# Performance work log

Hardware: AMD Instinct MI355X
Metric: run time of the kernel (lower is better)

The kernel has to match this reference:

```python
import jax, jax.numpy as jnp
import numpy as np

EPS = 1e-08
BASE_CR = 0.5
MIN_CR = 0.1


def _layernorm(h, g, b, eps=1e-5):
    m = jnp.mean(h, axis=-1, keepdims=True)
    v = jnp.mean((h - m) ** 2, axis=-1, keepdims=True)
    return (h - m) * jax.lax.rsqrt(v + eps) * g + b


def _normalize(h, eps=1e-12):
    n = jnp.sqrt(jnp.sum(h * h, axis=-1, keepdims=True))
    return h / jnp.maximum(n, eps)


def _conv1d(h, w, b):
    # h: [B,S,D], w: [K,I,O] (WIO), cross-correlation, SAME padding (torch Conv1d padding=1, k=3)
    y = jax.lax.conv_general_dilated(h, w, window_strides=(1,), padding='SAME',
                                     dimension_numbers=('NWC', 'WIO', 'NWC'))
    return y + b


def setup_inputs() -> dict:
    key = jax.random.key(0)
    ks = jax.random.split(key, 8)
    V, L, D, B, S = 50257, 2048, 1024, 8, 2048
    inp = {
        'x': jax.random.randint(ks[0], (B, S), 0, V),
        'token_emb': jax.random.normal(ks[1], (V, D), jnp.float32) * 0.02,
        'pos_emb': jax.random.normal(ks[2], (L, D), jnp.float32) * 0.02,
        'conv1_w': jax.random.normal(ks[3], (3, D, D), jnp.float32) * 0.025,
        'conv1_b': jnp.zeros((D,), jnp.float32),
        'conv2_w': jax.random.normal(ks[4], (3, D, D), jnp.float32) * 0.025,
        'conv2_b': jnp.zeros((D,), jnp.float32),
        'proj_w': jax.random.normal(ks[5], (D, D), jnp.float32) * 0.03,
        'proj_b': jnp.zeros((D,), jnp.float32),
        'ph_w': jax.random.normal(ks[6], (D, D), jnp.float32) * 0.03,
        'ph_b': jnp.zeros((D,), jnp.float32),
        'ln_g': jnp.ones((D,), jnp.float32),
        'ln_b': jnp.zeros((D,), jnp.float32),
    }
    return inp


def reference(x, token_emb, pos_emb, conv1_w, conv1_b, conv2_w, conv2_b,
              proj_w, proj_b, ph_w, ph_b, ln_g, ln_b):
    B, S = x.shape
    # token + position embedding
    h = token_emb[x] + pos_emb[:S][None, :, :]                 # [B,S,D]
    # two conv1d + gelu (exact erf, matching torch F.gelu default)
    h = jax.nn.gelu(_conv1d(h, conv1_w, conv1_b), approximate=False)
    h = jax.nn.gelu(_conv1d(h, conv2_w, conv2_b), approximate=False)
    h = _layernorm(h, ln_g, ln_b)
    # dropout is identity in eval mode
    # S is a power of two -> next_power_of_two(S) == S, no padding
    x_fft = jnp.fft.fft(h, axis=1)                              # [B,S,D] complex64
    magnitude = jnp.abs(x_fft)
    thresh = 0.1 * jnp.max(magnitude, axis=1, keepdims=True)
    complexity = jnp.mean((magnitude > thresh).astype(jnp.float32), axis=(1, 2))  # [B]
    cr = jnp.clip(BASE_CR * (1.0 - complexity), MIN_CR, 1.0)
    N = jnp.clip((cr * S).astype(jnp.int32), 1, S)              # [B] kept coefficients
    # vectorized ragged masking (replaces per-sample python loop/scatter)
    mask = (jnp.arange(S)[None, :] < N[:, None]).astype(jnp.float32)   # [B,S]
    x_fft_c = x_fft * mask[:, :, None]
    x_ifft_raw = jnp.fft.ifft(x_fft_c, n=S, axis=1).real        # [B,S,D]
    proj_out = x_ifft_raw @ proj_w + proj_b
    x_ifft = _layernorm(proj_out, ln_g, ln_b)
    recon_target = proj_out                                     # same proj of same ifft
    # loss
    cos_sim = jnp.sum(_normalize(x_ifft) * _normalize(recon_target), axis=-1)
    cos_sim = jnp.clip(cos_sim, -1.0 + EPS, 1.0 - EPS)
    d = x_ifft - recon_target
    l1 = jnp.where(jnp.abs(d) < 1.0, 0.5 * d * d, jnp.abs(d) - 0.5)    # smooth_l1, beta=1
    proj_x = x_ifft @ ph_w + ph_b
    proj_t = recon_target @ ph_w + ph_b
    sem = jnp.mean((_normalize(proj_x) - _normalize(proj_t)) ** 2, axis=-1)  # [B,S]
    combined = 0.6 * jnp.mean(1.0 - cos_sim) + 0.2 * jnp.mean(l1, axis=-1) + 0.2 * sem
    loss = jnp.sum(combined * mask) / (jnp.sum(mask) + EPS)
    return (x_ifft, loss)
```

## Files before the change

### kernel.cpp

```cpp
#include <hip/hip_runtime.h>
#include <math.h>

#define S_LEN 2048
#define D_DIM 1024
#define B_BATCH 8
#define R_ROWS (B_BATCH * S_LEN)
#define BD_ROWS (B_BATCH * D_DIM)
#define PAD_ROWS 2050

typedef unsigned short u16;
typedef unsigned int u32;
typedef __attribute__((ext_vector_type(8))) short bf16x8;
typedef __attribute__((ext_vector_type(4))) float f32x4;

__device__ __forceinline__ u16 f2bf(float f) {
    u32 x = __float_as_uint(f);
    u32 r = (x + 0x7fffu + ((x >> 16) & 1u)) >> 16;
    return (u16)r;
}
__device__ __forceinline__ float bf2f(u16 u) {
    return __uint_as_float(((u32)u) << 16);
}
__device__ __forceinline__ float gelu_exact(float x) {
    return 0.5f * x * (1.0f + erff(x * 0.70710678118654752f));
}
__device__ __forceinline__ int dr4(int v) {
    v = __brev((unsigned)v) >> 22;
    return ((v & 0x155) << 1) | ((v >> 1) & 0x155);
}
#define PIDX(i) ((i) + ((i) >> 5))

#define GLDS(gsrc, ldst)                                                                   \
    __builtin_amdgcn_global_load_lds(                                                      \
        (const __attribute__((address_space(1))) u32*)(gsrc),                              \
        (__attribute__((address_space(3))) u32*)(ldst), 16, 0, 0)

#define WAIT_LGKM0 do { asm volatile("s_waitcnt lgkmcnt(0)" ::: "memory");                 \
                        __builtin_amdgcn_sched_barrier(0); } while (0)
#define WAIT_VM(n)   do { asm volatile("s_waitcnt vmcnt(" #n ")" ::: "memory");            \
                          __builtin_amdgcn_sched_barrier(0); } while (0)

__global__ __launch_bounds__(256) void zero_pads(u16* __restrict__ P0, u16* __restrict__ P1)
{
    const int bid = blockIdx.x;
    u16* P = (bid >= 16) ? P1 : P0;
    const int ridx = bid & 15;
    const int b = ridx >> 1;
    const size_t row = (size_t)b * PAD_ROWS + (size_t)(ridx & 1) * (PAD_ROWS - 1);
    ((uint2*)(P + row * D_DIM))[threadIdx.x] = make_uint2(0u, 0u);
}

__global__ __launch_bounds__(256) void wconv(const float* __restrict__ W, u16* __restrict__ WT)
{
    __shared__ float t[32][33];
    const int tap = blockIdx.z;
    const int n0 = blockIdx.x * 32, k0 = blockIdx.y * 32;
    const int tx = threadIdx.x, ty = threadIdx.y;
    const float* ip = W + (size_t)tap * D_DIM * D_DIM;
    u16* op = WT + (size_t)tap * D_DIM * D_DIM;
#pragma unroll
    for (int u = 0; u < 4; u++)
        t[ty + u * 8][tx] = ip[(size_t)(k0 + ty + u * 8) * D_DIM + n0 + tx];
    __syncthreads();
#pragma unroll
    for (int u = 0; u < 4; u++)
        op[(size_t)(n0 + ty + u * 8) * D_DIM + k0 + tx] = f2bf(t[tx][ty + u * 8]);
}

__global__ __launch_bounds__(256) void wconv_inter(
    const float* __restrict__ W, const float* __restrict__ g, u16* __restrict__ WTI)
{
    __shared__ float t[32][33];
    const int n0 = blockIdx.x * 32, k0 = blockIdx.y * 32;
    const int tx = threadIdx.x, ty = threadIdx.y;
#pragma unroll
    for (int u = 0; u < 4; u++)
        t[ty + u * 8][tx] = W[(size_t)(k0 + ty + u * 8) * D_DIM + n0 + tx];
    __syncthreads();
    const float gk = g[k0 + tx];
#pragma unroll
    for (int u = 0; u < 4; u++) {
        const int n = n0 + ty + u * 8;
        const float w = t[tx][ty + u * 8];
        WTI[((size_t)(2 * n) << 10) + k0 + tx] = f2bf(w);
        WTI[((size_t)(2 * n + 1) << 10) + k0 + tx] = f2bf(w * gk);
    }
}

__global__ __launch_bounds__(256) void gemv_ph(
    const u16* __restrict__ WTI, const float* __restrict__ lnb,
    const float* __restrict__ phb, float* __restrict__ vg, float* __restrict__ c0)
{
    const int wid = threadIdx.x >> 6, lane = threadIdx.x & 63;
    const int n = blockIdx.x * 4 + wid;
    const u16* r0 = WTI + ((size_t)(2 * n) << 10) + lane * 16;
    const u16* r1 = WTI + ((size_t)(2 * n + 1) << 10) + lane * 16;
    float sb = 0.f, sg = 0.f;
#pragma unroll
    for (int h = 0; h < 2; h++) {
        uint4 w0 = *(const uint4*)(r0 + h * 8);
        uint4 w1 = *(const uint4*)(r1 + h * 8);
        float a[8], b8[8];
        a[0] = bf2f((u16)(w0.x & 0xffff)); a[1] = bf2f((u16)(w0.x >> 16));
        a[2] = bf2f((u16)(w0.y & 0xffff)); a[3] = bf2f((u16)(w0.y >> 16));
        a[4] = bf2f((u16)(w0.z & 0xffff)); a[5] = bf2f((u16)(w0.z >> 16));
        a[6] = bf2f((u16)(w0.w & 0xffff)); a[7] = bf2f((u16)(w0.w >> 16));
        b8[0] = bf2f((u16)(w1.x & 0xffff)); b8[1] = bf2f((u16)(w1.x >> 16));
        b8[2] = bf2f((u16)(w1.y & 0xffff)); b8[3] = bf2f((u16)(w1.y >> 16));
        b8[4] = bf2f((u16)(w1.z & 0xffff)); b8[5] = bf2f((u16)(w1.z >> 16));
        b8[6] = bf2f((u16)(w1.w & 0xffff)); b8[7] = bf2f((u16)(w1.w >> 16));
        const int kb = lane * 16 + h * 8;
        float4 l0 = *(const float4*)(lnb + kb), l1 = *(const float4*)(lnb + kb + 4);
        sb += a[0]*l0.x + a[1]*l0.y + a[2]*l0.z + a[3]*l0.w
            + a[4]*l1.x + a[5]*l1.y + a[6]*l1.z + a[7]*l1.w;
        sg += b8[0] + b8[1] + b8[2] + b8[3] + b8[4] + b8[5] + b8[6] + b8[7];
    }
#pragma unroll
    for (int off = 32; off > 0; off >>= 1) {
        sg += __shfl_xor(sg, off);
        sb += __shfl_xor(sb, off);
    }
    if (lane == 0) { vg[n] = sg; c0[n] = sb + phb[n]; }
}

__global__ __launch_bounds__(256) void emb_kernel(
    const int* __restrict__ x, const float* __restrict__ tok,
    const float* __restrict__ pos, u16* __restrict__ P0)
{
    const int row = blockIdx.x;
    const int tid = threadIdx.x;
    const int t = x[row];
    const int s = row & (S_LEN - 1);
    const int b = row >> 11;
    float4 a = ((const float4*)(tok + (size_t)t * D_DIM))[tid];
    float4 p = ((const float4*)(pos + (size_t)s * D_DIM))[tid];
    uint2 v;
    v.x = (u32)f2bf(a.x + p.x) | ((u32)f2bf(a.y + p.y) << 16);
    v.y = (u32)f2bf(a.z + p.z) | ((u32)f2bf(a.w + p.w) << 16);
    ((uint2*)(P0 + ((size_t)b * PAD_ROWS + 1 + s) * D_DIM))[tid] = v;
}

__global__ __launch_bounds__(512, 2) void gemm_8ph(
    const u16* __restrict__ A, const u16* __restrict__ WT,
    const float* __restrict__ bias,
    float* __restrict__ outF, u16* __restrict__ outB,
    int ntaps, int doGelu, int aPadded, int outBPadded)
{
    __shared__ u16 As[2][2][8192];
    __shared__ u16 Bs[2][2][8192];
    const int tid = threadIdx.x;
    const int wid = tid >> 6, lane = tid & 63;
    const int wm = wid >> 2, wn = wid & 3;
    const int l15 = lane & 15, l4 = lane >> 4;
    const int flat = blockIdx.y * 4 + blockIdx.x;
    const int xcd = flat & 7;
    const int ii = flat >> 3;
    const int by = xcd * 8 + (ii >> 2);
    const int bx = ii & 3;
    const int row0 = by * 256;
    const int col0 = bx * 256;
    const int b = row0 >> 11;
    const int srow0 = row0 & (S_LEN - 1);
    const int nt = ntaps * 16;
    const int NI = nt >> 1;

    const int stR = tid >> 2;
    const int stKc = (((tid & 3) ^ ((tid >> 3) & 3)) << 3);
    const int ldsOff = tid * 16;
    const int swz4 = ((l4 ^ ((l15 >> 1) & 3)) << 4);

#define STAGE_A(T_, s_) do {                                                               \
        const int tap_ = (T_) >> 4;                                                        \
        const int kb_ = ((T_) & 15) * 64 + (s_) * 32 + stKc;                               \
        const size_t ar_ = (aPadded ? (size_t)(b * PAD_ROWS + srow0 + tap_)                \
                                    : (size_t)row0);                                       \
        GLDS(A + ((ar_ + stR) << 10) + kb_,                                                \
             (char*)&As[(T_) & 1][s_][0] + ldsOff);                                        \
        GLDS(A + ((ar_ + stR + 128) << 10) + kb_,                                          \
             (char*)&As[(T_) & 1][s_][0] + ldsOff + 8192);                                 \
    } while (0)
#define STAGE_B(T_, s_) do {                                                               \
        const int tap_ = (T_) >> 4;                                                        \
        const int kb_ = ((T_) & 15) * 64 + (s_) * 32 + stKc;                               \
        const u16* wp_ = WT + ((size_t)tap_ << 20) + ((size_t)(col0 + stR) << 10) + kb_;   \
        GLDS(wp_, (char*)&Bs[(T_) & 1][s_][0] + ldsOff);                                   \
        GLDS(wp_ + (size_t)(128 << 10), (char*)&Bs[(T_) & 1][s_][0] + ldsOff + 8192);      \
    } while (0)
#define RD_A(dst_, buf_, s_, mih_) do {                                                    \
        const char* p_ = (const char*)&As[buf_][s_][0]                                     \
                         + (size_t)(wm * 128 + (mih_) * 64 + l15) * 64 + swz4;             \
        dst_[0] = *(const bf16x8*)(p_);                                                    \
        dst_[1] = *(const bf16x8*)(p_ + 1024);                                             \
        dst_[2] = *(const bf16x8*)(p_ + 2048);                                             \
        dst_[3] = *(const bf16x8*)(p_ + 3072);                                             \
    } while (0)
#define RD_B(dst_, buf_, s_) do {                                                          \
        const char* p_ = (const char*)&Bs[buf_][s_][0]                                     \
                         + (size_t)(wn * 64 + l15) * 64 + swz4;                            \
        dst_[0] = *(const bf16x8*)(p_);                                                    \
        dst_[1] = *(const bf16x8*)(p_ + 1024);                                             \
        dst_[2] = *(const bf16x8*)(p_ + 2048);                                             \
        dst_[3] = *(const bf16x8*)(p_ + 3072);                                             \
    } while (0)
#define MF(mih_, av_, bv_) do {                                                            \
        __builtin_amdgcn_s_setprio(1);                                                     \
        _Pragma("unroll")                                                                  \
        for (int mi_ = 0; mi_ < 4; mi_++)                                                  \
            _Pragma("unroll")                                                              \
            for (int ni_ = 0; ni_ < 4; ni_++)                                              \
                acc[(mih_) * 4 + mi_][ni_] = __builtin_amdgcn_mfma_f32_16x16x32_bf16(      \
                    av_[mi_], bv_[ni_], acc[(mih_) * 4 + mi_][ni_], 0, 0, 0);              \
        __builtin_amdgcn_s_setprio(0);                                                     \
    } while (0)
#define BAR __builtin_amdgcn_s_barrier()

    f32x4 acc[8][4];
#pragma unroll
    for (int m = 0; m < 8; m++)
#pragma unroll
        for (int n = 0; n < 4; n++) acc[m][n] = (f32x4){0.f, 0.f, 0.f, 0.f};

    STAGE_A(0, 0); STAGE_B(0, 0);
    STAGE_A(0, 1); STAGE_B(0, 1);
    STAGE_A(1, 0); STAGE_B(1, 0);
    WAIT_VM(4);
    BAR;

    for (int i = 0; i < NI; ++i) {
        const int o = 2 * i + 1;
        const int e2 = 2 * i + 2, o2 = 2 * i + 3;
        const bool last = (i == NI - 1);
        bf16x8 a[4], bv[4];
        RD_A(a, 0, 0, 0); RD_B(bv, 0, 0);
        STAGE_A(o, 1);
        BAR; WAIT_LGKM0;
        MF(0, a, bv);
        BAR;
        RD_A(a, 0, 0, 1);
        STAGE_B(o, 1);
        BAR; WAIT_LGKM0;
        MF(1, a, bv);
        BAR;
        RD_A(a, 0, 1, 0); RD_B(bv, 0, 1);
        if (!last) STAGE_A(e2, 0);
        BAR; WAIT_LGKM0;
        MF(0, a, bv);
        BAR;
        RD_A(a, 0, 1, 1);
        if (!last) STAGE_B(e2, 0);
        BAR; WAIT_LGKM0;
        MF(1, a, bv);
        if (last) { WAIT_VM(0); } else { WAIT_VM(4); }
        BAR;
        RD_A(a, 1, 0, 0); RD_B(bv, 1, 0);
        if (!last) STAGE_A(e2, 1);
        BAR; WAIT_LGKM0;
        MF(0, a, bv);
        BAR;
        RD_A(a, 1, 0, 1);
        if (!last) STAGE_B(e2, 1);
        BAR; WAIT_LGKM0;
        MF(1, a, bv);
        BAR;
        RD_A(a, 1, 1, 0); RD_B(bv, 1, 1);
        if (!last) STAGE_A(o2, 0);
        BAR; WAIT_LGKM0;
        MF(0, a, bv);
        BAR;
        RD_A(a, 1, 1, 1);
        if (!last) STAGE_B(o2, 0);
        BAR; WAIT_LGKM0;
        MF(1, a, bv);
        if (!last) { WAIT_VM(4); }
        BAR;
    }
#undef STAGE_A

    float bb[4];
#pragma unroll
    for (int ni = 0; ni < 4; ni++) bb[ni] = bias[col0 + wn * 64 + ni * 16 + l15];

#pragma unroll
    for (int mi = 0; mi < 8; mi++) {
#pragma unroll
        for (int ni = 0; ni < 4; ni++) {
#pragma unroll
            for (int reg = 0; reg < 4; reg++) {
                const int row = row0 + wm * 128 + mi * 16 + l4 * 4 + reg;
                const int col = col0 + wn * 64 + ni * 16 + l15;
                float v = acc[mi][ni][reg] + bb[ni];
                if (doGelu) v = gelu_exact(v);
                if (outF) outF[(size_t)row * D_DIM + col] = v;
                if (outB) {
                    const size_t orow = outBPadded
                        ? ((size_t)(row >> 11) * PAD_ROWS + 1 + (size_t)(row & (S_LEN - 1)))
                        : (size_t)row;
                    outB[orow * D_DIM + col] = f2bf(v);
                }
            }
        }
    }
}

__global__ __launch_bounds__(512, 2) void phstats_8ph(
    const u16* __restrict__ A, const u16* __restrict__ WTI,
    const float* __restrict__ phb, const float* __restrict__ vg,
    const float* __restrict__ c0, const float2* __restrict__ stats2,
    float* __restrict__ Sxx, float* __restrict__ Stt, float* __restrict__ Sxt)
{
    __shared__ u16 As[2][2][8192];
    __shared__ u16 Bs[2][2][8192];
    const int tid = threadIdx.x;
    const int wid = tid >> 6, lane = tid & 63;
    const int wm = wid >> 2, wn = wid & 3;
    const int l15 = lane & 15, l4 = lane >> 4;
    const int flat = blockIdx.y * 8 + blockIdx.x;
    const int xcd = flat & 7;
    const int ii = flat >> 3;
    const int by = xcd * 8 + (ii >> 3);
    const int bx = ii & 7;
    const int row0 = by * 256;
    const int col0 = bx * 256;
    const int NI = 8;

    const int stR = tid >> 2;
    const int stKc = (((tid & 3) ^ ((tid >> 3) & 3)) << 3);
    const int ldsOff = tid * 16;
    const int swz4 = ((l4 ^ ((l15 >> 1) & 3)) << 4);

#define STAGE_A(T_, s_) do {                                                               \
        const int kb_ = ((T_) & 15) * 64 + (s_) * 32 + stKc;                               \
        GLDS(A + (((size_t)row0 + stR) << 10) + kb_,                                       \
             (char*)&As[(T_) & 1][s_][0] + ldsOff);                                        \
        GLDS(A + (((size_t)row0 + stR + 128) << 10) + kb_,                                 \
             (char*)&As[(T_) & 1][s_][0] + ldsOff + 8192);                                 \
    } while (0)
#define STAGE_BI(T_, s_) do {                                                              \
        const int kb_ = ((T_) & 15) * 64 + (s_) * 32 + stKc;                               \
        const u16* wp_ = WTI + ((size_t)(col0 + stR) << 10) + kb_;                         \
        GLDS(wp_, (char*)&Bs[(T_) & 1][s_][0] + ldsOff);                                   \
        GLDS(wp_ + (size_t)(128 << 10), (char*)&Bs[(T_) & 1][s_][0] + ldsOff + 8192);      \
    } while (0)

    f32x4 acc[8][4];
#pragma unroll
    for (int m = 0; m < 8; m++)
#pragma unroll
        for (int n = 0; n < 4; n++) acc[m][n] = (f32x4){0.f, 0.f, 0.f, 0.f};

    STAGE_A(0, 0); STAGE_BI(0, 0);
    STAGE_A(0, 1); STAGE_BI(0, 1);
    STAGE_A(1, 0); STAGE_BI(1, 0);
    WAIT_VM(4);
    BAR;

    for (int i = 0; i < NI; ++i) {
        const int o = 2 * i + 1;
        const int e2 = 2 * i + 2, o2 = 2 * i + 3;
        const bool last = (i == NI - 1);
        bf16x8 a[4], bv[4];
        RD_A(a, 0, 0, 0); RD_B(bv, 0, 0);
        STAGE_A(o, 1);
        BAR; WAIT_LGKM0;
        MF(0, a, bv);
        BAR;
        RD_A(a, 0, 0, 1);
        STAGE_BI(o, 1);
        BAR; WAIT_LGKM0;
        MF(1, a, bv);
        BAR;
        RD_A(a, 0, 1, 0); RD_B(bv, 0, 1);
        if (!last) STAGE_A(e2, 0);
        BAR; WAIT_LGKM0;
        MF(0, a, bv);
        BAR;
        RD_A(a, 0, 1, 1);
        if (!last) STAGE_BI(e2, 0);
        BAR; WAIT_LGKM0;
        MF(1, a, bv);
        if (last) { WAIT_VM(0); } else { WAIT_VM(4); }
        BAR;
        RD_A(a, 1, 0, 0); RD_B(bv, 1, 0);
        if (!last) STAGE_A(e2, 1);
        BAR; WAIT_LGKM0;
        MF(0, a, bv);
        BAR;
        RD_A(a, 1, 0, 1);
        if (!last) STAGE_BI(e2, 1);
        BAR; WAIT_LGKM0;
        MF(1, a, bv);
        BAR;
        RD_A(a, 1, 1, 0); RD_B(bv, 1, 1);
        if (!last) STAGE_A(o2, 0);
        BAR; WAIT_LGKM0;
        MF(0, a, bv);
        BAR;
        RD_A(a, 1, 1, 1);
        if (!last) STAGE_BI(o2, 0);
        BAR; WAIT_LGKM0;
        MF(1, a, bv);
        if (!last) { WAIT_VM(4); }
        BAR;
    }
#undef STAGE_A
#undef STAGE_BI
#undef RD_A
#undef RD_B
#undef MF
#undef BAR

    float phv[4], vgv[4], c0v[4];
#pragma unroll
    for (int ni = 0; ni < 4; ni++) {
        const int col = col0 + wn * 64 + ni * 16 + l15;
        const int j = col >> 1;
        phv[ni] = phb[j]; vgv[ni] = vg[j]; c0v[ni] = c0[j];
    }
    const bool odd = (l15 & 1) != 0;
#pragma unroll
    for (int mi = 0; mi < 8; mi++) {
#pragma unroll
        for (int reg = 0; reg < 4; reg++) {
            const int row = row0 + wm * 128 + mi * 16 + l4 * 4 + reg;
            const float2 st = stats2[row];
            const float mrs = st.x * st.y;
            float sxx = 0.f, stt = 0.f, sxt = 0.f;
#pragma unroll
            for (int ni = 0; ni < 4; ni++) {
                const float raw = acc[mi][ni][reg];
                const float val = odd ? (st.y * raw - mrs * vgv[ni] + c0v[ni])
                                      : (raw + phv[ni]);
                const float par = __shfl_xor(val, 1);
                const float pt = odd ? par : val;
                const float px = odd ? val : par;
                stt = fmaf(pt, pt, stt);
                sxx = fmaf(px, px, sxx);
                sxt = fmaf(pt, px, sxt);
            }
#pragma unroll
            for (int off = 1; off < 16; off <<= 1) {
                sxx += __shfl_xor(sxx, off);
                stt += __shfl_xor(stt, off);
                sxt += __shfl_xor(sxt, off);
            }
            if (l15 == 0) {
                atomicAdd(&Sxx[row], 0.5f * sxx);
                atomicAdd(&Stt[row], 0.5f * stt);
                atomicAdd(&Sxt[row], 0.5f * sxt);
            }
        }
    }
}

__global__ __launch_bounds__(256) void ln_stats(
    const u16* __restrict__ in, float2* __restrict__ stats)
{
    const int row = blockIdx.x;
    const int tid = threadIdx.x;
    uint2 raw = ((const uint2*)(in + (size_t)row * D_DIM))[tid];
    float v0 = bf2f((u16)(raw.x & 0xffff)), v1 = bf2f((u16)(raw.x >> 16));
    float v2 = bf2f((u16)(raw.y & 0xffff)), v3 = bf2f((u16)(raw.y >> 16));
    float s = v0 + v1 + v2 + v3;
    float s2 = v0 * v0 + v1 * v1 + v2 * v2 + v3 * v3;
#pragma unroll
    for (int off = 32; off > 0; off >>= 1) {
        s += __shfl_xor(s, off);
        s2 += __shfl_xor(s2, off);
    }
    __shared__ float red[8];
    if ((tid & 63) == 0) { red[(tid >> 6) * 2] = s; red[(tid >> 6) * 2 + 1] = s2; }
    __syncthreads();
    if (tid == 0) {
        s = red[0] + red[2] + red[4] + red[6];
        s2 = red[1] + red[3] + red[5] + red[7];
        const float m = s * (1.0f / D_DIM);
        const float var = s2 * (1.0f / D_DIM) - m * m;
        stats[row] = make_float2(m, rsqrtf(var + 1e-5f));
    }
}

__global__ __launch_bounds__(256) void transposeLN(
    const u16* __restrict__ in, const float2* __restrict__ stats,
    const float* __restrict__ g, const float* __restrict__ beta,
    float* __restrict__ out)
{
    __shared__ float t[32][33];
    const int b = blockIdx.z;
    const int n0 = blockIdx.x * 32, m0 = blockIdx.y * 32;
    const int tx = threadIdx.x, ty = threadIdx.y;
    const u16* ip = in + (size_t)b * S_LEN * D_DIM;
    float* op = out + (size_t)b * S_LEN * D_DIM;
#pragma unroll
    for (int u = 0; u < 4; u++)
        t[ty + u * 8][tx] = bf2f(ip[(size_t)(m0 + ty + u * 8) * D_DIM + n0 + tx]);
    __syncthreads();
    const float2 st = stats[b * S_LEN + m0 + tx];
#pragma unroll
    for (int u = 0; u < 4; u++) {
        const int d = n0 + ty + u * 8;
        const float val = (t[tx][ty + u * 8] - st.x) * st.y * g[d] + beta[d];
        op[(size_t)d * S_LEN + m0 + tx] = val;
    }
}

__global__ __launch_bounds__(256) void fft_fwd(
    const float* __restrict__ in, float2* __restrict__ X, int* __restrict__ counts)
{
    __shared__ float re[1056], im[1056], twr[1024], twi[1024];
    __shared__ float redf[4];
    __shared__ int redi[4];
    const int tid = threadIdx.x;
    const int row = blockIdx.x;
    const float2* src = (const float2*)(in + (size_t)row * S_LEN);
#pragma unroll
    for (int u = 0; u < 4; u++) {
        int e = tid + u * 256;
        float ang = -3.14159265358979f * (float)e * (1.0f / 512.0f);
        float sn, cs; __sincosf(ang, &sn, &cs);
        twr[e] = cs; twi[e] = sn;
    }
#pragma unroll
    for (int u = 0; u < 4; u++) {
        int t = tid + u * 256;
        float2 z = src[t];
        int p = PIDX(dr4(t));
        re[p] = z.x; im[p] = z.y;
    }
    __syncthreads();
#pragma unroll
    for (int s = 1; s <= 5; ++s) {
        const int mq = 1 << (2 * (s - 1));
        const int fsh = 2 * (5 - s);
        const int j = tid & (mq - 1);
        const int g = tid >> (2 * (s - 1));
        const int i0 = (g << (2 * s)) + j;
        const int e1 = j << fsh;
        const int p0 = PIDX(i0), p1 = PIDX(i0 + mq), p2 = PIDX(i0 + 2 * mq), p3 = PIDX(i0 + 3 * mq);
        float a0r = re[p0], a0i = im[p0];
        float a1r = re[p1], a1i = im[p1];
        float a2r = re[p2], a2i = im[p2];
        float a3r = re[p3], a3i = im[p3];
        float w1r = twr[e1], w1i = twi[e1];
        float w2r = twr[2 * e1], w2i = twi[2 * e1];
        float w3r = twr[3 * e1], w3i = twi[3 * e1];
        float b1r = a1r * w1r - a1i * w1i, b1i = a1r * w1i + a1i * w1r;
        float b2r = a2r * w2r - a2i * w2i, b2i = a2r * w2i + a2i * w2r;
        float b3r = a3r * w3r - a3i * w3i, b3i = a3r * w3i + a3i * w3r;
        float t0r = a0r + b2r, t0i = a0i + b2i;
        float t1r = a0r - b2r, t1i = a0i - b2i;
        float t2r = b1r + b3r, t2i = b1i + b3i;
        float t3r = b1r - b3r, t3i = b1i - b3i;
        re[p0] = t0r + t2r; im[p0] = t0i + t2i;
        re[p2] = t0r - t2r; im[p2] = t0i - t2i;
        re[p1] = t1r + t3i; im[p1] = t1i - t3r;
        re[p3] = t1r - t3i; im[p3] = t1i + t3r;
        __syncthreads();
    }
    float2* dst = X + (size_t)row * 1024;
    float mag[4];
    float xtra = 0.0f;
    float lmax = 0.0f;
#pragma unroll
    for (int u = 0; u < 4; u++) {
        int k = tid + u * 256;
        int mk = (1024 - k) & 1023;
        float rk = re[PIDX(k)], ik = im[PIDX(k)];
        float rm = re[PIDX(mk)], imm = im[PIDX(mk)];
        float er = 0.5f * (rk + rm);
        float ei = 0.5f * (ik - imm);
        float orr = 0.5f * (ik + imm);
        float oii = -0.5f * (rk - rm);
        float ang = -3.14159265358979f * (float)k * (1.0f / 1024.0f);
        float sn, cs; __sincosf(ang, &sn, &cs);
        float xr = er + orr * cs - oii * sn;
        float xi = ei + orr * sn + oii * cs;
        dst[k] = make_float2(xr, xi);
        float m2 = xr * xr + xi * xi;
        mag[u] = m2;
        lmax = fmaxf(lmax, m2);
        if (k == 0) {
            float x1024 = re[PIDX(0)] - im[PIDX(0)];
            xtra = x1024 * x1024;
            lmax = fmaxf(lmax, xtra);
        }
    }
#pragma unroll
    for (int off = 32; off > 0; off >>= 1) lmax = fmaxf(lmax, __shfl_xor(lmax, off));
    if ((tid & 63) == 0) redf[tid >> 6] = lmax;
    __syncthreads();
    const float bmax = fmaxf(fmaxf(redf[0], redf[1]), fmaxf(redf[2], redf[3]));
    const float thr = 0.01f * bmax;
    int lc = 0;
#pragma unroll
    for (int u = 0; u < 4; u++) {
        int k = tid + u * 256;
        lc += (mag[u] > thr) ? ((k == 0) ? 1 : 2) : 0;
    }
    if (tid == 0) lc += (xtra > thr) ? 1 : 0;
#pragma unroll
    for (int off = 32; off > 0; off >>= 1) lc += __shfl_xor(lc, off);
    if ((tid & 63) == 0) redi[tid >> 6] = lc;
    __syncthreads();
    if (tid == 0)
        atomicAdd(&counts[(row >> 10) * 64 + (row & 63)],
                  redi[0] + redi[1] + redi[2] + redi[3]);
}

__global__ void calc_n(const int* __restrict__ counts, int* __restrict__ Ndev)
{
    const int t = threadIdx.x;
    for (int b = 0; b < B_BATCH; b++) {
        int c = counts[b * 64 + t];
#pragma unroll
        for (int off = 32; off > 0; off >>= 1) c += __shfl_xor(c, off);
        if (t == 0) {
            float cf = (float)c * (1.0f / 2097152.0f);
            float cr = 0.5f * (1.0f - cf);
            cr = fminf(fmaxf(cr, 0.1f), 1.0f);
            int n = (int)(cr * 2048.0f);
            n = n < 1 ? 1 : (n > S_LEN ? S_LEN : n);
            Ndev[b] = n;
        }
    }
}

__global__ __launch_bounds__(256) void fft_inv(
    const float2* __restrict__ X, const int* __restrict__ Ndev,
    u16* __restrict__ outb)
{
    __shared__ float re[1056], im[1056], twr[1024], twi[1024];
    const int tid = threadIdx.x;
    const int row = blockIdx.x;
    const int Nb = Ndev[row >> 10];
    const float2* src = X + (size_t)row * 1024;
#pragma unroll
    for (int u = 0; u < 4; u++) {
        int e = tid + u * 256;
        float ang = 3.14159265358979f * (float)e * (1.0f / 512.0f);
        float sn, cs; __sincosf(ang, &sn, &cs);
        twr[e] = cs; twi[e] = sn;
    }
#pragma unroll
    for (int u = 0; u < 4; u++) {
        int k = tid + u * 256;
        float Ar = 0.f, Ai = 0.f, Br = 0.f, Bi = 0.f;
        if (k == 0) {
            float2 h = src[0];
            Ar = h.x; Ai = h.y;
        } else {
            if (k < Nb) { float2 h = src[k]; Ar = 0.5f * h.x; Ai = 0.5f * h.y; }
            int km = 1024 - k;
            if (km < Nb) { float2 h = src[km]; Br = 0.5f * h.x; Bi = -0.5f * h.y; }
        }
        float ang = 3.14159265358979f * (float)k * (1.0f / 1024.0f);
        float sn, cs; __sincosf(ang, &sn, &cs);
        float drr = Ar - Br, dri = Ai - Bi;
        float Dr = drr * cs - dri * sn;
        float Di = drr * sn + dri * cs;
        float Cr = (Ar + Br) - Di;
        float Ci = (Ai + Bi) + Dr;
        int p = PIDX(dr4(k));
        re[p] = Cr; im[p] = Ci;
    }
    __syncthreads();
#pragma unroll
    for (int s = 1; s <= 4; ++s) {
        const int mq = 1 << (2 * (s - 1));
        const int fsh = 2 * (5 - s);
        const int j = tid & (mq - 1);
        const int g = tid >> (2 * (s - 1));
        const int i0 = (g << (2 * s)) + j;
        const int e1 = j << fsh;
        const int p0 = PIDX(i0), p1 = PIDX(i0 + mq), p2 = PIDX(i0 + 2 * mq), p3 = PIDX(i0 + 3 * mq);
        float a0r = re[p0], a0i = im[p0];
        float a1r = re[p1], a1i = im[p1];
        float a2r = re[p2], a2i = im[p2];
        float a3r = re[p3], a3i = im[p3];
        float w1r = twr[e1], w1i = twi[e1];
        float w2r = twr[2 * e1], w2i = twi[2 * e1];
        float w3r = twr[3 * e1], w3i = twi[3 * e1];
        float b1r = a1r * w1r - a1i * w1i, b1i = a1r * w1i + a1i * w1r;
        float b2r = a2r * w2r - a2i * w2i, b2i = a2r * w2i + a2i * w2r;
        float b3r = a3r * w3r - a3i * w3i, b3i = a3r * w3i + a3i * w3r;
        float t0r = a0r + b2r, t0i = a0i + b2i;
        float t1r = a0r - b2r, t1i = a0i - b2i;
        float t2r = b1r + b3r, t2i = b1i + b3i;
        float t3r = b1r - b3r, t3i = b1i - b3i;
        re[p0] = t0r + t2r; im[p0] = t0i + t2i;
        re[p2] = t0r - t2r; im[p2] = t0i - t2i;
        re[p1] = t1r - t3i; im[p1] = t1i + t3r;
        re[p3] = t1r + t3i; im[p3] = t1i - t3r;
        __syncthreads();
    }
    {
        const int j = tid;
        const int e1 = j;
        const int p0 = PIDX(j), p1 = PIDX(j + 256), p2 = PIDX(j + 512), p3 = PIDX(j + 768);
        float a0r = re[p0], a0i = im[p0];
        float a1r = re[p1], a1i = im[p1];
        float a2r = re[p2], a2i = im[p2];
        float a3r = re[p3], a3i = im[p3];
        float w1r = twr[e1], w1i = twi[e1];
        float w2r = twr[2 * e1], w2i = twi[2 * e1];
        float w3r = twr[3 * e1], w3i = twi[3 * e1];
        float b1r = a1r * w1r - a1i * w1i, b1i = a1r * w1i + a1i * w1r;
        float b2r = a2r * w2r - a2i * w2i, b2i = a2r * w2i + a2i * w2r;
        float b3r = a3r * w3r - a3i * w3i, b3i = a3r * w3i + a3i * w3r;
        float t0r = a0r + b2r, t0i = a0i + b2i;
        float t1r = a0r - b2r, t1i = a0i - b2i;
        float t2r = b1r + b3r, t2i = b1i + b3i;
        float t3r = b1r - b3r, t3i = b1i - b3i;
        const float sc = 1.0f / 2048.0f;
        u32* dst = (u32*)(outb + (size_t)row * S_LEN);
        dst[j]       = (u32)f2bf((t0r + t2r) * sc) | ((u32)f2bf((t0i + t2i) * sc) << 16);
        dst[j + 256] = (u32)f2bf((t1r - t3i) * sc) | ((u32)f2bf((t1i + t3r) * sc) << 16);
        dst[j + 512] = (u32)f2bf((t0r - t2r) * sc) | ((u32)f2bf((t0i - t2i) * sc) << 16);
        dst[j + 768] = (u32)f2bf((t1r + t3i) * sc) | ((u32)f2bf((t1i - t3r) * sc) << 16);
    }
}

__global__ __launch_bounds__(256) void transpose_bb(
    const u16* __restrict__ in, u16* __restrict__ out, int M, int N)
{
    __shared__ u16 t[32][33];
    const int b = blockIdx.z;
    const int n0 = blockIdx.x * 32, m0 = blockIdx.y * 32;
    const int tx = threadIdx.x, ty = threadIdx.y;
    const u16* ip = in + (size_t)b * M * N;
    u16* op = out + (size_t)b * M * N;
#pragma unroll
    for (int u = 0; u < 4; u++)
        t[ty + u * 8][tx] = ip[(size_t)(m0 + ty + u * 8) * N + n0 + tx];
    __syncthreads();
#pragma unroll
    for (int u = 0; u < 4; u++)
        op[(size_t)(n0 + ty + u * 8) * M + m0 + tx] = t[tx][ty + u * 8];
}

__global__ __launch_bounds__(256) void ln_loss(
    const float* __restrict__ in, const float* __restrict__ g,
    const float* __restrict__ beta, float* __restrict__ outF,
    float2* __restrict__ stats2,
    float* __restrict__ rowA, float* __restrict__ rowL1)
{
    const int row = blockIdx.x;
    const int tid = threadIdx.x;
    float4 v = ((const float4*)(in + (size_t)row * D_DIM))[tid];
    float s = v.x + v.y + v.z + v.w;
    float s2 = v.x * v.x + v.y * v.y + v.z * v.z + v.w * v.w;
#pragma unroll
    for (int off = 32; off > 0; off >>= 1) {
        s += __shfl_xor(s, off);
        s2 += __shfl_xor(s2, off);
    }
    __shared__ float red[8];
    if ((tid & 63) == 0) { red[(tid >> 6) * 2] = s; red[(tid >> 6) * 2 + 1] = s2; }
    __syncthreads();
    s = red[0] + red[2] + red[4] + red[6];
    s2 = red[1] + red[3] + red[5] + red[7];
    const float m = s * (1.0f / D_DIM);
    const float var = s2 * (1.0f / D_DIM) - m * m;
    const float rs = rsqrtf(var + 1e-5f);
    float4 gg = ((const float4*)g)[tid];
    float4 bb = ((const float4*)beta)[tid];
    float4 o;
    o.x = (v.x - m) * rs * gg.x + bb.x;
    o.y = (v.y - m) * rs * gg.y + bb.y;
    o.z = (v.z - m) * rs * gg.z + bb.z;
    o.w = (v.w - m) * rs * gg.w + bb.w;
    ((float4*)(outF + (size_t)row * D_DIM))[tid] = o;

    float xx = o.x * o.x + o.y * o.y + o.z * o.z + o.w * o.w;
    float rr = v.x * v.x + v.y * v.y + v.z * v.z + v.w * v.w;
    float xr = o.x * v.x + o.y * v.y + o.z * v.z + o.w * v.w;
    float l1 = 0.f;
    {
        float d, ad;
        d = o.x - v.x; ad = fabsf(d); l1 += (ad < 1.0f) ? 0.5f * d * d : ad - 0.5f;
        d = o.y - v.y; ad = fabsf(d); l1 += (ad < 1.0f) ? 0.5f * d * d : ad - 0.5f;
        d = o.z - v.z; ad = fabsf(d); l1 += (ad < 1.0f) ? 0.5f * d * d : ad - 0.5f;
        d = o.w - v.w; ad = fabsf(d); l1 += (ad < 1.0f) ? 0.5f * d * d : ad - 0.5f;
    }
#pragma unroll
    for (int off = 32; off > 0; off >>= 1) {
        xx += __shfl_xor(xx, off); rr += __shfl_xor(rr, off);
        xr += __shfl_xor(xr, off); l1 += __shfl_xor(l1, off);
    }
    __shared__ float red2[4][4];
    __syncthreads();
    if ((tid & 63) == 0) {
        int w = tid >> 6;
        red2[w][0] = xx; red2[w][1] = rr; red2[w][2] = xr; red2[w][3] = l1;
    }
    __syncthreads();
    if (tid == 0) {
        stats2[row] = make_float2(m, rs);
        xx = red2[0][0] + red2[1][0] + red2[2][0] + red2[3][0];
        rr = red2[0][1] + red2[1][1] + red2[2][1] + red2[3][1];
        xr = red2[0][2] + red2[1][2] + red2[2][2] + red2[3][2];
        l1 = red2[0][3] + red2[1][3] + red2[2][3] + red2[3][3];
        float nx = fmaxf(sqrtf(xx), 1e-12f);
        float nr = fmaxf(sqrtf(rr), 1e-12f);
        float cs = xr / (nx * nr);
        cs = fminf(fmaxf(cs, -1.0f + 1e-8f), 1.0f - 1e-8f);
        rowA[row] = 1.0f - cs;
        rowL1[row] = l1;
    }
}

__global__ __launch_bounds__(1024) void final_loss(
    const float* __restrict__ rowA, const float* __restrict__ rowL1,
    const float* __restrict__ Sxx, const float* __restrict__ Stt,
    const float* __restrict__ Sxt,
    const int* __restrict__ Ndev, float* __restrict__ out)
{
    const int tid = threadIdx.x;
    float sa = 0.f, sb = 0.f;
#pragma unroll
    for (int i = 0; i < 16; i++) {
        int r = tid + i * 1024;
        sa += rowA[r];
        int b = r >> 11, s = r & (S_LEN - 1);
        if (s < Ndev[b]) {
            float sx = Sxx[r], st = Stt[r], sxtv = Sxt[r];
            float nxx = fmaxf(sqrtf(sx), 1e-12f);
            float ntt = fmaxf(sqrtf(st), 1e-12f);
            float sem = (sx / (nxx * nxx) + st / (ntt * ntt)
                         - 2.0f * sxtv / (nxx * ntt)) * (1.0f / D_DIM);
            sb += 0.2f * (rowL1[r] * (1.0f / D_DIM)) + 0.2f * sem;
        }
    }
#pragma unroll
    for (int off = 32; off > 0; off >>= 1) {
        sa += __shfl_xor(sa, off);
        sb += __shfl_xor(sb, off);
    }
    __shared__ float ra[16], rb[16];
    if ((tid & 63) == 0) { ra[tid >> 6] = sa; rb[tid >> 6] = sb; }
    __syncthreads();
    if (tid == 0) {
        float A = 0.f, Bs = 0.f;
#pragma unroll
        for (int i = 0; i < 16; i++) { A += ra[i]; Bs += rb[i]; }
        int K = 0;
        for (int b = 0; b < B_BATCH; b++) K += Ndev[b];
        float Kf = (float)K;
        float M = A * (1.0f / 16384.0f);
        out[(size_t)R_ROWS * D_DIM] = (0.6f * M * Kf + Bs) / (Kf + 1e-8f);
    }
}

extern "C" void kernel_launch(void* const* d_in, const int* in_sizes, int n_in,
                              void* d_out, int out_size, void* d_ws, size_t ws_size,
                              hipStream_t stream)
{
    (void)in_sizes; (void)n_in; (void)out_size; (void)ws_size;
    const int*   x       = (const int*)  d_in[0];
    const float* tok     = (const float*)d_in[1];
    const float* pos     = (const float*)d_in[2];
    const float* conv1_w = (const float*)d_in[3];
    const float* conv1_b = (const float*)d_in[4];
    const float* conv2_w = (const float*)d_in[5];
    const float* conv2_b = (const float*)d_in[6];
    const float* proj_w  = (const float*)d_in[7];
    const float* proj_b  = (const float*)d_in[8];
    const float* ph_w    = (const float*)d_in[9];
    const float* ph_b    = (const float*)d_in[10];
    const float* ln_g    = (const float*)d_in[11];
    const float* ln_b    = (const float*)d_in[12];
    float* out = (float*)d_out;

    char* ws = (char*)d_ws;
    int*    counts = (int*)(ws);
    int*    Ndev   = (int*)(ws + 2048);
    float2* stats  = (float2*)(ws + 4096);
    float2* stats2 = (float2*)(ws + 135168);
    float*  Sxx    = (float*)(ws + 266240);
    float*  Stt    = (float*)(ws + 331776);
    float*  Sxt    = (float*)(ws + 397312);
    float*  rowA   = (float*)(ws + 462848);
    float*  rowL1  = (float*)(ws + 528384);
    float*  vg     = (float*)(ws + 593920);
    float*  c0     = (float*)(ws + 598016);
    const size_t MB = 1ull << 20;
    u16*   WT   = (u16*)(ws + 1 * MB);
    u16*   WTI  = WT;
    u16*   P0   = (u16*)(ws + 17 * MB);
    u16*   P1   = (u16*)(ws + 50 * MB);
    float* F32A = (float*)(ws + 83 * MB);
    float* F32B = (float*)(ws + 148 * MB);

    hipMemsetAsync(ws, 0, MB, stream);
    zero_pads<<<32, 256, 0, stream>>>(P0, P1);
    wconv<<<dim3(32, 32, 3), dim3(32, 8), 0, stream>>>(conv1_w, WT);
    wconv<<<dim3(32, 32, 3), dim3(32, 8), 0, stream>>>(conv2_w, WT + 3u * (1u << 20));
    wconv<<<dim3(32, 32, 1), dim3(32, 8), 0, stream>>>(proj_w, WT + 6u * (1u << 20));
    emb_kernel<<<R_ROWS, 256, 0, stream>>>(x, tok, pos, P0);
    gemm_8ph<<<dim3(4, 64), 512, 0, stream>>>(P0, WT, conv1_b,
                                              nullptr, P1, 3, 1, 1, 1);
    wconv_inter<<<dim3(32, 32, 1), dim3(32, 8), 0, stream>>>(ph_w, ln_g, WTI);
    gemv_ph<<<256, 256, 0, stream>>>(WTI, ln_b, ph_b, vg, c0);
    gemm_8ph<<<dim3(4, 64), 512, 0, stream>>>(P1, WT + 3u * (1u << 20), conv2_b,
                                              nullptr, P0, 3, 1, 1, 0);
    ln_stats<<<R_ROWS, 256, 0, stream>>>(P0, stats);
    transposeLN<<<dim3(32, 64, 8), dim3(32, 8), 0, stream>>>(P0, stats, ln_g, ln_b, F32B);
    fft_fwd<<<BD_ROWS, 256, 0, stream>>>(F32B, (float2*)F32A, counts);
    calc_n<<<1, 64, 0, stream>>>(counts, Ndev);
    fft_inv<<<BD_ROWS, 256, 0, stream>>>((const float2*)F32A, Ndev, P1);
    transpose_bb<<<dim3(64, 32, 8), dim3(32, 8), 0, stream>>>(P1, P0, D_DIM, S_LEN);
    gemm_8ph<<<dim3(4, 64), 512, 0, stream>>>(P0, WT + 6u * (1u << 20), proj_b,
                                              F32A, P1, 1, 0, 0, 0);
    ln_loss<<<R_ROWS, 256, 0, stream>>>(F32A, ln_g, ln_b, out, stats2, rowA, rowL1);
    phstats_8ph<<<dim3(8, 64), 512, 0, stream>>>(P1, WTI, ph_b, vg, c0, stats2,
                                                 Sxx, Stt, Sxt);
    final_loss<<<1, 1024, 0, stream>>>(rowA, rowL1, Sxx, Stt, Sxt, Ndev, out);
}
```

Before: 603.2 us.

## Fuse LayerNorm row statistics into GEMM epilogues and store FFT spectrum as bf16

```diff
diff --git a/kernel.cpp b/kernel.cpp
--- a/kernel.cpp
+++ b/kernel.cpp
@@ -144,6 +144,7 @@
     const u16* __restrict__ A, const u16* __restrict__ WT,
     const float* __restrict__ bias,
     float* __restrict__ outF, u16* __restrict__ outB,
+    float* __restrict__ rowS, float* __restrict__ rowQ,
     int ntaps, int doGelu, int aPadded, int outBPadded)
 {
     __shared__ u16 As[2][2][8192];
@@ -283,10 +284,11 @@
 #pragma unroll
     for (int mi = 0; mi < 8; mi++) {
 #pragma unroll
-        for (int ni = 0; ni < 4; ni++) {
-#pragma unroll
-            for (int reg = 0; reg < 4; reg++) {
-                const int row = row0 + wm * 128 + mi * 16 + l4 * 4 + reg;
+        for (int reg = 0; reg < 4; reg++) {
+            const int row = row0 + wm * 128 + mi * 16 + l4 * 4 + reg;
+            float s_ = 0.f, q_ = 0.f;
+#pragma unroll
+            for (int ni = 0; ni < 4; ni++) {
                 const int col = col0 + wn * 64 + ni * 16 + l15;
                 float v = acc[mi][ni][reg] + bb[ni];
                 if (doGelu) v = gelu_exact(v);
@@ -297,6 +299,18 @@
                         : (size_t)row;
                     outB[orow * D_DIM + col] = f2bf(v);
                 }
+                if (rowS) { s_ += v; q_ = fmaf(v, v, q_); }
+            }
+            if (rowS) {
+#pragma unroll
+                for (int off = 1; off < 16; off <<= 1) {
+                    s_ += __shfl_xor(s_, off);
+                    q_ += __shfl_xor(q_, off);
+                }
+                if (l15 == 0) {
+                    atomicAdd(&rowS[row], s_);
+                    atomicAdd(&rowQ[row], q_);
+                }
             }
         }
     }
@@ -305,7 +319,8 @@
 __global__ __launch_bounds__(512, 2) void phstats_8ph(
     const u16* __restrict__ A, const u16* __restrict__ WTI,
     const float* __restrict__ phb, const float* __restrict__ vg,
-    const float* __restrict__ c0, const float2* __restrict__ stats2,
+    const float* __restrict__ c0,
+    const float* __restrict__ rowS2, const float* __restrict__ rowQ2,
     float* __restrict__ Sxx, float* __restrict__ Stt, float* __restrict__ Sxt)
 {
     __shared__ u16 As[2][2][8192];
@@ -422,13 +437,15 @@
 #pragma unroll
         for (int reg = 0; reg < 4; reg++) {
             const int row = row0 + wm * 128 + mi * 16 + l4 * 4 + reg;
-            const float2 st = stats2[row];
-            const float mrs = st.x * st.y;
+            const float mS = rowS2[row] * (1.0f / D_DIM);
+            const float var = rowQ2[row] * (1.0f / D_DIM) - mS * mS;
+            const float rsv = rsqrtf(var + 1e-5f);
+            const float mrs = mS * rsv;
             float sxx = 0.f, stt = 0.f, sxt = 0.f;
 #pragma unroll
             for (int ni = 0; ni < 4; ni++) {
                 const float raw = acc[mi][ni][reg];
-                const float val = odd ? (st.y * raw - mrs * vgv[ni] + c0v[ni])
+                const float val = odd ? (rsv * raw - mrs * vgv[ni] + c0v[ni])
                                       : (raw + phv[ni]);
                 const float par = __shfl_xor(val, 1);
                 const float pt = odd ? par : val;
@@ -452,35 +469,9 @@
     }
 }
 
-__global__ __launch_bounds__(256) void ln_stats(
-    const u16* __restrict__ in, float2* __restrict__ stats)
-{
-    const int row = blockIdx.x;
-    const int tid = threadIdx.x;
-    uint2 raw = ((const uint2*)(in + (size_t)row * D_DIM))[tid];
-    float v0 = bf2f((u16)(raw.x & 0xffff)), v1 = bf2f((u16)(raw.x >> 16));
-    float v2 = bf2f((u16)(raw.y & 0xffff)), v3 = bf2f((u16)(raw.y >> 16));
-    float s = v0 + v1 + v2 + v3;
-    float s2 = v0 * v0 + v1 * v1 + v2 * v2 + v3 * v3;
-#pragma unroll
-    for (int off = 32; off > 0; off >>= 1) {
-        s += __shfl_xor(s, off);
-        s2 += __shfl_xor(s2, off);
-    }
-    __shared__ float red[8];
-    if ((tid & 63) == 0) { red[(tid >> 6) * 2] = s; red[(tid >> 6) * 2 + 1] = s2; }
-    __syncthreads();
-    if (tid == 0) {
-        s = red[0] + red[2] + red[4] + red[6];
-        s2 = red[1] + red[3] + red[5] + red[7];
-        const float m = s * (1.0f / D_DIM);
-        const float var = s2 * (1.0f / D_DIM) - m * m;
-        stats[row] = make_float2(m, rsqrtf(var + 1e-5f));
-    }
-}
-
 __global__ __launch_bounds__(256) void transposeLN(
-    const u16* __restrict__ in, const float2* __restrict__ stats,
+    const u16* __restrict__ in, const float* __restrict__ rowS,
+    const float* __restrict__ rowQ,
     const float* __restrict__ g, const float* __restrict__ beta,
     float* __restrict__ out)
 {
@@ -494,17 +485,20 @@
     for (int u = 0; u < 4; u++)
         t[ty + u * 8][tx] = bf2f(ip[(size_t)(m0 + ty + u * 8) * D_DIM + n0 + tx]);
     __syncthreads();
-    const float2 st = stats[b * S_LEN + m0 + tx];
+    const int row = b * S_LEN + m0 + tx;
+    const float mS = rowS[row] * (1.0f / D_DIM);
+    const float var = rowQ[row] * (1.0f / D_DIM) - mS * mS;
+    const float rs = rsqrtf(var + 1e-5f);
 #pragma unroll
     for (int u = 0; u < 4; u++) {
         const int d = n0 + ty + u * 8;
-        const float val = (t[tx][ty + u * 8] - st.x) * st.y * g[d] + beta[d];
+        const float val = (t[tx][ty + u * 8] - mS) * rs * g[d] + beta[d];
         op[(size_t)d * S_LEN + m0 + tx] = val;
     }
 }
 
 __global__ __launch_bounds__(256) void fft_fwd(
-    const float* __restrict__ in, float2* __restrict__ X, int* __restrict__ counts)
+    const float* __restrict__ in, u32* __restrict__ X, int* __restrict__ counts)
 {
     __shared__ float re[1056], im[1056], twr[1024], twi[1024];
     __shared__ float redf[4];
@@ -556,7 +550,7 @@
         re[p3] = t1r - t3i; im[p3] = t1i + t3r;
         __syncthreads();
     }
-    float2* dst = X + (size_t)row * 1024;
+    u32* dst = X + (size_t)row * 1024;
     float mag[4];
     float xtra = 0.0f;
     float lmax = 0.0f;
@@ -574,7 +568,7 @@
         float sn, cs; __sincosf(ang, &sn, &cs);
         float xr = er + orr * cs - oii * sn;
         float xi = ei + orr * sn + oii * cs;
-        dst[k] = make_float2(xr, xi);
+        dst[k] = (u32)f2bf(xr) | ((u32)f2bf(xi) << 16);
         float m2 = xr * xr + xi * xi;
         mag[u] = m2;
         lmax = fmaxf(lmax, m2);
@@ -625,14 +619,14 @@
 }
 
 __global__ __launch_bounds__(256) void fft_inv(
-    const float2* __restrict__ X, const int* __restrict__ Ndev,
+    const u32* __restrict__ X, const int* __restrict__ Ndev,
     u16* __restrict__ outb)
 {
     __shared__ float re[1056], im[1056], twr[1024], twi[1024];
     const int tid = threadIdx.x;
     const int row = blockIdx.x;
     const int Nb = Ndev[row >> 10];
-    const float2* src = X + (size_t)row * 1024;
+    const u32* src = X + (size_t)row * 1024;
 #pragma unroll
     for (int u = 0; u < 4; u++) {
         int e = tid + u * 256;
@@ -645,12 +639,20 @@
         int k = tid + u * 256;
         float Ar = 0.f, Ai = 0.f, Br = 0.f, Bi = 0.f;
         if (k == 0) {
-            float2 h = src[0];
-            Ar = h.x; Ai = h.y;
+            u32 w = src[0];
+            Ar = bf2f((u16)(w & 0xffff)); Ai = bf2f((u16)(w >> 16));
         } else {
-            if (k < Nb) { float2 h = src[k]; Ar = 0.5f * h.x; Ai = 0.5f * h.y; }
+            if (k < Nb) {
+                u32 w = src[k];
+                Ar = 0.5f * bf2f((u16)(w & 0xffff));
+                Ai = 0.5f * bf2f((u16)(w >> 16));
+            }
             int km = 1024 - k;
-            if (km < Nb) { float2 h = src[km]; Br = 0.5f * h.x; Bi = -0.5f * h.y; }
+            if (km < Nb) {
+                u32 w = src[km];
+                Br = 0.5f * bf2f((u16)(w & 0xffff));
+                Bi = -0.5f * bf2f((u16)(w >> 16));
+            }
         }
         float ang = 3.14159265358979f * (float)k * (1.0f / 1024.0f);
         float sn, cs; __sincosf(ang, &sn, &cs);
@@ -738,48 +740,38 @@
 }
 
 __global__ __launch_bounds__(256) void ln_loss(
-    const float* __restrict__ in, const float* __restrict__ g,
+    const u16* __restrict__ in, const float* __restrict__ g,
     const float* __restrict__ beta, float* __restrict__ outF,
-    float2* __restrict__ stats2,
+    const float* __restrict__ rowS2, const float* __restrict__ rowQ2,
     float* __restrict__ rowA, float* __restrict__ rowL1)
 {
     const int row = blockIdx.x;
     const int tid = threadIdx.x;
-    float4 v = ((const float4*)(in + (size_t)row * D_DIM))[tid];
-    float s = v.x + v.y + v.z + v.w;
-    float s2 = v.x * v.x + v.y * v.y + v.z * v.z + v.w * v.w;
-#pragma unroll
-    for (int off = 32; off > 0; off >>= 1) {
-        s += __shfl_xor(s, off);
-        s2 += __shfl_xor(s2, off);
-    }
-    __shared__ float red[8];
-    if ((tid & 63) == 0) { red[(tid >> 6) * 2] = s; red[(tid >> 6) * 2 + 1] = s2; }
-    __syncthreads();
-    s = red[0] + red[2] + red[4] + red[6];
-    s2 = red[1] + red[3] + red[5] + red[7];
-    const float m = s * (1.0f / D_DIM);
-    const float var = s2 * (1.0f / D_DIM) - m * m;
+    uint2 raw = ((const uint2*)(in + (size_t)row * D_DIM))[tid];
+    float v0 = bf2f((u16)(raw.x & 0xffff)), v1 = bf2f((u16)(raw.x >> 16));
+    float v2 = bf2f((u16)(raw.y & 0xffff)), v3 = bf2f((u16)(raw.y >> 16));
+    const float m = rowS2[row] * (1.0f / D_DIM);
+    const float var = rowQ2[row] * (1.0f / D_DIM) - m * m;
     const float rs = rsqrtf(var + 1e-5f);
     float4 gg = ((const float4*)g)[tid];
     float4 bb = ((const float4*)beta)[tid];
     float4 o;
-    o.x = (v.x - m) * rs * gg.x + bb.x;
-    o.y = (v.y - m) * rs * gg.y + bb.y;
-    o.z = (v.z - m) * rs * gg.z + bb.z;
-    o.w = (v.w - m) * rs * gg.w + bb.w;
+    o.x = (v0 - m) * rs * gg.x + bb.x;
+    o.y = (v1 - m) * rs * gg.y + bb.y;
+    o.z = (v2 - m) * rs * gg.z + bb.z;
+    o.w = (v3 - m) * rs * gg.w + bb.w;
     ((float4*)(outF + (size_t)row * D_DIM))[tid] = o;
 
     float xx = o.x * o.x + o.y * o.y + o.z * o.z + o.w * o.w;
-    float rr = v.x * v.x + v.y * v.y + v.z * v.z + v.w * v.w;
-    float xr = o.x * v.x + o.y * v.y + o.z * v.z + o.w * v.w;
+    float rr = v0 * v0 + v1 * v1 + v2 * v2 + v3 * v3;
+    float xr = o.x * v0 + o.y * v1 + o.z * v2 + o.w * v3;
     float l1 = 0.f;
     {
         float d, ad;
-        d = o.x - v.x; ad = fabsf(d); l1 += (ad < 1.0f) ? 0.5f * d * d : ad - 0.5f;
-        d = o.y - v.y; ad = fabsf(d); l1 += (ad < 1.0f) ? 0.5f * d * d : ad - 0.5f;
-        d = o.z - v.z; ad = fabsf(d); l1 += (ad < 1.0f) ? 0.5f * d * d : ad - 0.5f;
-        d = o.w - v.w; ad = fabsf(d); l1 += (ad < 1.0f) ? 0.5f * d * d : ad - 0.5f;
+        d = o.x - v0; ad = fabsf(d); l1 += (ad < 1.0f) ? 0.5f * d * d : ad - 0.5f;
+        d = o.y - v1; ad = fabsf(d); l1 += (ad < 1.0f) ? 0.5f * d * d : ad - 0.5f;
+        d = o.z - v2; ad = fabsf(d); l1 += (ad < 1.0f) ? 0.5f * d * d : ad - 0.5f;
+        d = o.w - v3; ad = fabsf(d); l1 += (ad < 1.0f) ? 0.5f * d * d : ad - 0.5f;
     }
 #pragma unroll
     for (int off = 32; off > 0; off >>= 1) {
@@ -787,14 +779,12 @@
         xr += __shfl_xor(xr, off); l1 += __shfl_xor(l1, off);
     }
     __shared__ float red2[4][4];
-    __syncthreads();
     if ((tid & 63) == 0) {
         int w = tid >> 6;
         red2[w][0] = xx; red2[w][1] = rr; red2[w][2] = xr; red2[w][3] = l1;
     }
     __syncthreads();
     if (tid == 0) {
-        stats2[row] = make_float2(m, rs);
         xx = red2[0][0] + red2[1][0] + red2[2][0] + red2[3][0];
         rr = red2[0][1] + red2[1][1] + red2[2][1] + red2[3][1];
         xr = red2[0][2] + red2[1][2] + red2[2][2] + red2[3][2];
@@ -873,8 +863,6 @@
     char* ws = (char*)d_ws;
     int*    counts = (int*)(ws);
     int*    Ndev   = (int*)(ws + 2048);
-    float2* stats  = (float2*)(ws + 4096);
-    float2* stats2 = (float2*)(ws + 135168);
     float*  Sxx    = (float*)(ws + 266240);
     float*  Stt    = (float*)(ws + 331776);
     float*  Sxt    = (float*)(ws + 397312);
@@ -882,12 +870,16 @@
     float*  rowL1  = (float*)(ws + 528384);
     float*  vg     = (float*)(ws + 593920);
     float*  c0     = (float*)(ws + 598016);
+    float*  rowS   = (float*)(ws + 602112);
+    float*  rowQ   = (float*)(ws + 667648);
+    float*  rowS2  = (float*)(ws + 733184);
+    float*  rowQ2  = (float*)(ws + 798720);
     const size_t MB = 1ull << 20;
     u16*   WT   = (u16*)(ws + 1 * MB);
     u16*   WTI  = WT;
     u16*   P0   = (u16*)(ws + 17 * MB);
     u16*   P1   = (u16*)(ws + 50 * MB);
-    float* F32A = (float*)(ws + 83 * MB);
+    u32*   Xs   = (u32*)(ws + 83 * MB);
     float* F32B = (float*)(ws + 148 * MB);
 
     hipMemsetAsync(ws, 0, MB, stream);
@@ -897,21 +889,21 @@
     wconv<<<dim3(32, 32, 1), dim3(32, 8), 0, stream>>>(proj_w, WT + 6u * (1u << 20));
     emb_kernel<<<R_ROWS, 256, 0, stream>>>(x, tok, pos, P0);
     gemm_8ph<<<dim3(4, 64), 512, 0, stream>>>(P0, WT, conv1_b,
-                                              nullptr, P1, 3, 1, 1, 1);
+                                              nullptr, P1, nullptr, nullptr, 3, 1, 1, 1);
     wconv_inter<<<dim3(32, 32, 1), dim3(32, 8), 0, stream>>>(ph_w, ln_g, WTI);
     gemv_ph<<<256, 256, 0, stream>>>(WTI, ln_b, ph_b, vg, c0);
     gemm_8ph<<<dim3(4, 64), 512, 0, stream>>>(P1, WT + 3u * (1u << 20), conv2_b,
-                                              nullptr, P0, 3, 1, 1, 0);
-    ln_stats<<<R_ROWS, 256, 0, stream>>>(P0, stats);
-    transposeLN<<<dim3(32, 64, 8), dim3(32, 8), 0, stream>>>(P0, stats, ln_g, ln_b, F32B);
-    fft_fwd<<<BD_ROWS, 256, 0, stream>>>(F32B, (float2*)F32A, counts);
+                                              nullptr, P0, rowS, rowQ, 3, 1, 1, 0);
+    transposeLN<<<dim3(32, 64, 8), dim3(32, 8), 0, stream>>>(P0, rowS, rowQ,
+                                                             ln_g, ln_b, F32B);
+    fft_fwd<<<BD_ROWS, 256, 0, stream>>>(F32B, Xs, counts);
     calc_n<<<1, 64, 0, stream>>>(counts, Ndev);
-    fft_inv<<<BD_ROWS, 256, 0, stream>>>((const float2*)F32A, Ndev, P1);
+    fft_inv<<<BD_ROWS, 256, 0, stream>>>(Xs, Ndev, P1);
     transpose_bb<<<dim3(64, 32, 8), dim3(32, 8), 0, stream>>>(P1, P0, D_DIM, S_LEN);
     gemm_8ph<<<dim3(4, 64), 512, 0, stream>>>(P0, WT + 6u * (1u << 20), proj_b,
-                                              F32A, P1, 1, 0, 0, 0);
-    ln_loss<<<R_ROWS, 256, 0, stream>>>(F32A, ln_g, ln_b, out, stats2, rowA, rowL1);
-    phstats_8ph<<<dim3(8, 64), 512, 0, stream>>>(P1, WTI, ph_b, vg, c0, stats2,
-                                                 Sxx, Stt, Sxt);
+                                              nullptr, P1, rowS2, rowQ2, 1, 0, 0, 0);
+    ln_loss<<<R_ROWS, 256, 0, stream>>>(P1, ln_g, ln_b, out, rowS2, rowQ2, rowA, rowL1);
+    phstats_8ph<<<dim3(8, 64), 512, 0, stream>>>(P1, WTI, ph_b, vg, c0,
+                                                 rowS2, rowQ2, Sxx, Stt, Sxt);
     final_loss<<<1, 1024, 0, stream>>>(rowA, rowL1, Sxx, Stt, Sxt, Ndev, out);
 }
```

Result: no change. 593.7 us (-1.6%).
